# Kernel tuning notes

Hardware: AMD Instinct MI355X
Metric: run time of the kernel (lower is better)

## Reference

```python
import jax, jax.numpy as jnp
import numpy as np
from jax import lax

D_MODEL = 1024; N_HEADS = 16; D_FF = 4096
D_INNER = 2048; D_STATE = 16; D_CONV = 4; DT_RANK = 64
B = 4; T = 1024; TF = 512
HD = D_MODEL // N_HEADS


def setup_inputs() -> dict:
    key = jax.random.key(0)
    ks = jax.random.split(key, 24)
    r = lambda i, shape, s=0.02: jax.random.normal(ks[i], shape, jnp.float32) * s
    lengths = jnp.array([512, 384, 448, 320])
    styled_mask = jnp.arange(TF)[None, :] < lengths[:, None]  # True = valid
    inp = {
        'x': jax.random.normal(ks[0], (B, T, D_MODEL), jnp.float32),
        'styled_frames': jax.random.normal(ks[1], (B, TF, D_MODEL), jnp.float32),
        'styled_mask': styled_mask,
        'ln1_g': jnp.ones((D_MODEL,)), 'ln1_b': jnp.zeros((D_MODEL,)),
        'ln2_g': jnp.ones((D_MODEL,)), 'ln2_b': jnp.zeros((D_MODEL,)),
        'ln3_g': jnp.ones((D_MODEL,)), 'ln3_b': jnp.zeros((D_MODEL,)),
        'm_in_w': r(2, (D_MODEL, 2 * D_INNER)),
        'm_conv_w': r(3, (D_INNER, D_CONV), 0.1),
        'm_conv_b': jnp.zeros((D_INNER,)),
        'm_xproj_w': r(4, (D_INNER, DT_RANK + 2 * D_STATE)),
        'm_dt_w': r(5, (DT_RANK, D_INNER), 0.1),
        'm_dt_b': jnp.full((D_INNER,), -4.6),  # softplus -> dt ~ 0.01
        'm_A_log': jnp.log(jnp.broadcast_to(jnp.arange(1, D_STATE + 1, dtype=jnp.float32), (D_INNER, D_STATE))),
        'm_D': jnp.ones((D_INNER,)),
        'm_out_w': r(6, (D_INNER, D_MODEL)),
        'attn_in_w': r(7, (3 * D_MODEL, D_MODEL)),
        'attn_in_b': jnp.zeros((3 * D_MODEL,)),
        'attn_out_w': r(8, (D_MODEL, D_MODEL)),
        'attn_out_b': jnp.zeros((D_MODEL,)),
        'ff_w1': r(9, (D_MODEL, D_FF)),
        'ff_b1': jnp.zeros((D_FF,)),
        'ff_w2': r(10, (D_FF, D_MODEL)),
        'ff_b2': jnp.zeros((D_MODEL,)),
    }
    return inp


def _layer_norm(x, g, b):
    m = x.mean(-1, keepdims=True)
    v = ((x - m) ** 2).mean(-1, keepdims=True)
    return (x - m) / jnp.sqrt(v + 1e-5) * g + b


def _mamba(h, m_in_w, m_conv_w, m_conv_b, m_xproj_w, m_dt_w, m_dt_b, m_A_log, m_D, m_out_w):
    xz = h @ m_in_w                                   # (B,T,2*d_inner)
    xm, z = jnp.split(xz, 2, axis=-1)
    # causal depthwise conv1d
    xt = jnp.pad(xm.transpose(0, 2, 1), ((0, 0), (0, 0), (D_CONV - 1, 0)))  # (B,d_inner,T+pad)
    xc = lax.conv_general_dilated(xt, m_conv_w[:, None, :], (1,), 'VALID',
                                  feature_group_count=D_INNER,
                                  dimension_numbers=('NCH', 'OIH', 'NCH'))
    xc = jax.nn.silu(xc + m_conv_b[None, :, None]).transpose(0, 2, 1)       # (B,T,d_inner)
    x_dbl = xc @ m_xproj_w
    dt, Bs, Cs = jnp.split(x_dbl, [DT_RANK, DT_RANK + D_STATE], axis=-1)
    dt = jax.nn.softplus(dt @ m_dt_w + m_dt_b)        # (B,T,d_inner)
    A = -jnp.exp(m_A_log)                             # (d_inner,d_state)

    def step(hs, inp):
        dt_t, B_t, C_t, u_t = inp                     # (B,d_inner),(B,d_state),(B,d_state),(B,d_inner)
        dA = jnp.exp(dt_t[:, :, None] * A)            # (B,d_inner,d_state)
        hs = dA * hs + dt_t[:, :, None] * B_t[:, None, :] * u_t[:, :, None]
        y = jnp.einsum('bds,bs->bd', hs, C_t)
        return hs, y

    h0 = jnp.zeros((xc.shape[0], D_INNER, D_STATE), xc.dtype)
    inputs = (dt.transpose(1, 0, 2), Bs.transpose(1, 0, 2), Cs.transpose(1, 0, 2), xc.transpose(1, 0, 2))
    hT, ys = lax.scan(step, h0, inputs)
    y = ys.transpose(1, 0, 2) + xc * m_D
    y = y * jax.nn.silu(z)
    return y @ m_out_w, hT


def _cross_attn(q_in, kv_in, valid_mask, in_w, in_b, out_w, out_b):
    d = D_MODEL
    q = q_in @ in_w[:d].T + in_b[:d]
    k = kv_in @ in_w[d:2 * d].T + in_b[d:2 * d]
    v = kv_in @ in_w[2 * d:].T + in_b[2 * d:]
    q = q.reshape(q.shape[0], q.shape[1], N_HEADS, HD)
    k = k.reshape(k.shape[0], k.shape[1], N_HEADS, HD)
    v = v.reshape(v.shape[0], v.shape[1], N_HEADS, HD)
    scores = jnp.einsum('bqhd,bkhd->bhqk', q, k) / np.sqrt(HD)
    scores = jnp.where(valid_mask[:, None, None, :], scores, jnp.finfo(scores.dtype).min)
    attn = jax.nn.softmax(scores, axis=-1)
    o = jnp.einsum('bhqk,bkhd->bqhd', attn, v).reshape(q_in.shape)
    return o @ out_w.T + out_b


def reference(x, styled_frames, styled_mask,
              ln1_g, ln1_b, ln2_g, ln2_b, ln3_g, ln3_b,
              m_in_w, m_conv_w, m_conv_b, m_xproj_w, m_dt_w, m_dt_b, m_A_log, m_D, m_out_w,
              attn_in_w, attn_in_b, attn_out_w, attn_out_b,
              ff_w1, ff_b1, ff_w2, ff_b2):
    h = _layer_norm(x, ln1_g, ln1_b)
    h_mamba, new_state = _mamba(h, m_in_w, m_conv_w, m_conv_b, m_xproj_w, m_dt_w, m_dt_b, m_A_log, m_D, m_out_w)
    x = x + h_mamba
    h = _layer_norm(x, ln2_g, ln2_b)
    x = x + _cross_attn(h, styled_frames, styled_mask, attn_in_w, attn_in_b, attn_out_w, attn_out_b)
    h = _layer_norm(x, ln3_g, ln3_b)
    ff = jax.nn.gelu(h @ ff_w1 + ff_b1, approximate=False) @ ff_w2 + ff_b2
    x = x + ff
    return x, new_state
```

## Files before the change

### kernel.cpp

```cpp
#include <hip/hip_runtime.h>
#include <hip/hip_bf16.h>
#include <cstdint>

using bf16 = __hip_bfloat16;

typedef __attribute__((ext_vector_type(8))) short short8;
typedef __attribute__((ext_vector_type(4))) float floatx4;

__device__ __forceinline__ float b2f(bf16 h) { return __bfloat162float(h); }
__device__ __forceinline__ bf16 f2b(float f) { return __float2bfloat16(f); }
__device__ __forceinline__ float uitf(unsigned u) { union { unsigned u; float f; } c; c.u = u; return c.f; }

__device__ __forceinline__ void async16(const bf16* g, bf16* l) {
    __builtin_amdgcn_global_load_lds(
        (const __attribute__((address_space(1))) uint32_t*)(const void*)g,
        (__attribute__((address_space(3))) uint32_t*)(void*)l, 16, 0, 0);
}

__global__ void lens_flag_kernel(const unsigned char* __restrict__ mask,
                                 const unsigned int* __restrict__ ln1g_raw,
                                 int* __restrict__ hdr) {
    __shared__ int cnt[4];
    int tid = threadIdx.x;
    if (tid < 4) cnt[tid] = 0;
    __syncthreads();
    unsigned char b0 = mask[0], b1 = mask[1];
    int width = (b1 == 0) ? 4 : ((b0 == 1) ? 1 : 2);
    if (width == 4) {
        const unsigned int* m = (const unsigned int*)mask;
        for (int i = tid; i < 2048; i += 256) if (m[i] != 0u) atomicAdd(&cnt[i >> 9], 1);
    } else if (width == 2) {
        const unsigned short* m = (const unsigned short*)mask;
        for (int i = tid; i < 2048; i += 256) if (m[i] != 0u) atomicAdd(&cnt[i >> 9], 1);
    } else {
        for (int i = tid; i < 2048; i += 256) if (mask[i] != 0u) atomicAdd(&cnt[i >> 9], 1);
    }
    __syncthreads();
    if (tid < 4) hdr[tid] = cnt[tid];
    if (tid == 4) hdr[4] = (ln1g_raw[0] == 0x3F800000u) ? 1 : 0;
}

__global__ void convert_kernel(const void* __restrict__ src, bf16* __restrict__ dst, int n,
                               const int* __restrict__ flagp) {
    int i = blockIdx.x * 256 + threadIdx.x;
    if (i >= n) return;
    if (*flagp) dst[i] = f2b(((const float*)src)[i]);
    else        dst[i] = ((const bf16*)src)[i];
}

struct SmallSrcs { const void* p[15]; };
__global__ void convert_smalls_kernel(SmallSrcs s, bf16* __restrict__ dst,
                                      const int* __restrict__ flagp) {
    const int ends[16] = {0, 1024, 2048, 3072, 4096, 5120, 6144, 14336, 16384, 18432,
                          51200, 53248, 56320, 57344, 61440, 62464};
    int i = blockIdx.x * 256 + threadIdx.x;
    if (i >= 62464) return;
    int seg = 0;
    #pragma unroll
    for (int k = 1; k < 16; ++k) if (i >= ends[k]) seg = k;
    int local = i - ends[seg];
    const void* sp = s.p[seg];
    if (*flagp) dst[i] = f2b(((const float*)sp)[local]);
    else        dst[i] = ((const bf16*)sp)[local];
}

__global__ void transpose_any(const void* __restrict__ src, bf16* __restrict__ dst,
                              int R, int C, const int* __restrict__ flagp) {
    __shared__ bf16 tile[32][33];
    bool f32 = (*flagp != 0);
    int bx = blockIdx.x * 32, by = blockIdx.y * 32;
    int tx = threadIdx.x;
    for (int i = threadIdx.y; i < 32; i += 8) {
        int y = by + i, x = bx + tx;
        if (y < R && x < C) {
            size_t idx = (size_t)y * C + x;
            tile[i][tx] = f32 ? f2b(((const float*)src)[idx]) : ((const bf16*)src)[idx];
        }
    }
    __syncthreads();
    for (int i = threadIdx.y; i < 32; i += 8) {
        int yo = bx + i, xo = by + tx;
        if (yo < C && xo < R) dst[(size_t)yo * R + xo] = tile[tx][i];
    }
}

__global__ void vtrans_kernel(const bf16* __restrict__ kv, bf16* __restrict__ vt) {
    __shared__ bf16 t[32][33];
    int kc = blockIdx.x * 32, dc = blockIdx.y * 32;
    int bh = blockIdx.z; int b = bh >> 4, h = bh & 15;
    int tx = threadIdx.x;
    for (int i = threadIdx.y; i < 32; i += 8)
        t[i][tx] = kv[(size_t)(b * 512 + kc + i) * 2048 + 1024 + h * 64 + dc + tx];
    __syncthreads();
    for (int i = threadIdx.y; i < 32; i += 8)
        vt[(size_t)(bh * 64 + dc + i) * 512 + kc + tx] = t[tx][i];
}

__global__ __launch_bounds__(256) void ln_kernel(const bf16* __restrict__ x, const bf16* __restrict__ g,
                                                 const bf16* __restrict__ bb, bf16* __restrict__ out) {
    int row = blockIdx.x, tid = threadIdx.x;
    const bf16* xr = x + (size_t)row * 1024;
    float v[4];
    {
        uint2 raw = *(const uint2*)(xr + tid * 4);
        v[0] = uitf(raw.x << 16); v[1] = uitf(raw.x & 0xffff0000u);
        v[2] = uitf(raw.y << 16); v[3] = uitf(raw.y & 0xffff0000u);
    }
    float sum = v[0] + v[1] + v[2] + v[3];
    float sq = v[0]*v[0] + v[1]*v[1] + v[2]*v[2] + v[3]*v[3];
    for (int off = 32; off; off >>= 1) { sum += __shfl_xor(sum, off); sq += __shfl_xor(sq, off); }
    __shared__ float wsm[8];
    int wave = tid >> 6;
    if ((tid & 63) == 0) { wsm[wave * 2] = sum; wsm[wave * 2 + 1] = sq; }
    __syncthreads();
    sum = wsm[0] + wsm[2] + wsm[4] + wsm[6];
    sq  = wsm[1] + wsm[3] + wsm[5] + wsm[7];
    float mean = sum * (1.f / 1024.f);
    float var = sq * (1.f / 1024.f) - mean * mean;
    float rstd = rsqrtf(var + 1e-5f);
    bf16* orow = out + (size_t)row * 1024;
    #pragma unroll
    for (int c = 0; c < 4; ++c) {
        int col = tid * 4 + c;
        orow[col] = f2b((v[c] - mean) * rstd * b2f(g[col]) + b2f(bb[col]));
    }
}

template<int BN>
__global__ __launch_bounds__(256) void gemm_bt(
    const bf16* __restrict__ A, int lda,
    const bf16* __restrict__ Bt, int ldb,
    void* __restrict__ Cp, int ldc, int c_f32,
    int M, int N, int K,
    const bf16* __restrict__ bias,
    const bf16* __restrict__ res, int ldres,
    int act)
{
    constexpr int NJ = BN / 32;
    __shared__ __align__(16) bf16 As[3][128 * 32];
    __shared__ __align__(16) bf16 Bs[3][BN * 32];
    const int tid = threadIdx.x;
    const int lane = tid & 63;
    const int wave = tid >> 6;
    const int wr = (wave >> 1) * 64;
    const int wc = (wave & 1) * (BN / 2);
    const int lrow = lane & 15;
    const int quad = lane >> 4;

    const int gx = gridDim.x;
    const int nwg = gx * gridDim.y;
    const int orig = blockIdx.y * gx + blockIdx.x;
    int wgid = orig;
    if ((nwg & 7) == 0) wgid = (orig & 7) * (nwg >> 3) + (orig >> 3);
    const int n0 = (wgid % gx) * BN;
    const int m0 = (wgid / gx) * 128;

    const int r0 = tid >> 2;
    const int c0 = (((tid & 3) ^ ((r0 >> 1) & 3)) << 3);

    floatx4 acc[4][NJ];
    #pragma unroll
    for (int i = 0; i < 4; ++i)
        #pragma unroll
        for (int j = 0; j < NJ; ++j) acc[i][j] = (floatx4){0.f, 0.f, 0.f, 0.f};

    const int n1 = n0 + r0, n2 = n0 + r0 + 64;
    const bool fullN = (n0 + BN <= N);
    const bool bok1 = n1 < N, bok2 = n2 < N;
    const int4 z4 = {0, 0, 0, 0};

    const bf16* Ag1 = A + (size_t)(m0 + r0) * lda + c0;
    const bf16* Ag2 = A + (size_t)(m0 + r0 + 64) * lda + c0;
    const bf16* Bg1 = Bt + (size_t)n1 * ldb + c0;
    const bf16* Bg2 = Bt + (size_t)n2 * ldb + c0;

    const int chsw = ((quad ^ ((lrow >> 1) & 3)) << 3);
    const int nt = K >> 5;

    if (fullN) {
        auto stage = [&](int buf, int k0) {
            bf16* AsW = &As[buf][tid * 8];
            bf16* BsW = &Bs[buf][tid * 8];
            async16(Ag1 + k0, AsW);
            async16(Ag2 + k0, AsW + 64 * 32);
            async16(Bg1 + k0, BsW);
            if constexpr (BN == 128) async16(Bg2 + k0, BsW + 64 * 32);
        };
        const unsigned asB0 = (unsigned)(uintptr_t)(void*)&As[0][0];
        const unsigned bsB0 = (unsigned)(uintptr_t)(void*)&Bs[0][0];
        unsigned aoff[4], boff[NJ];
        #pragma unroll
        for (int i = 0; i < 4; ++i) aoff[i] = asB0 + (unsigned)(((wr + i * 16 + lrow) * 32 + chsw) * 2);
        #pragma unroll
        for (int j = 0; j < NJ; ++j) boff[j] = bsB0 + (unsigned)(((wc + j * 16 + lrow) * 32 + chsw) * 2);

        stage(0, 0);
        if (nt > 1) stage(1, 32);
        int cur = 0;
        for (int t = 0; t < nt; ++t) {
            if (t + 1 < nt) {
                if constexpr (BN == 128) asm volatile("s_waitcnt vmcnt(4)" ::: "memory");
                else                     asm volatile("s_waitcnt vmcnt(3)" ::: "memory");
            } else {
                asm volatile("s_waitcnt vmcnt(0)" ::: "memory");
            }
            __builtin_amdgcn_s_barrier();
            __builtin_amdgcn_sched_barrier(0);
            if (t + 2 < nt) {
                int nb = cur + 2; if (nb >= 3) nb -= 3;
                stage(nb, (t + 2) << 5);
            }
            const unsigned abuf = (unsigned)(cur * 128 * 32 * 2);
            const unsigned bbuf = (unsigned)(cur * BN * 32 * 2);
            short8 af[4], bfr[NJ];
            #pragma unroll
            for (int i = 0; i < 4; ++i)
                asm volatile("ds_read_b128 %0, %1" : "=v"(af[i]) : "v"(aoff[i] + abuf));
            #pragma unroll
            for (int j = 0; j < NJ; ++j)
                asm volatile("ds_read_b128 %0, %1" : "=v"(bfr[j]) : "v"(boff[j] + bbuf));
            asm volatile("s_waitcnt lgkmcnt(0)" ::: "memory");
            __builtin_amdgcn_sched_barrier(0);
            #pragma unroll
            for (int i = 0; i < 4; ++i)
                #pragma unroll
                for (int j = 0; j < NJ; ++j)
                    acc[i][j] = __builtin_amdgcn_mfma_f32_16x16x32_bf16(af[i], bfr[j], acc[i][j], 0, 0, 0);
            if (++cur == 3) cur = 0;
        }
    } else {
        bf16* AsW = &As[0][tid * 8];
        bf16* BsW = &Bs[0][tid * 8];
        for (int k0 = 0; k0 < K; k0 += 32) {
            __syncthreads();
            async16(Ag1 + k0, AsW);
            async16(Ag2 + k0, AsW + 64 * 32);
            *(int4*)BsW = bok1 ? *(const int4*)(Bg1 + k0) : z4;
            if constexpr (BN == 128)
                *(int4*)(BsW + 64 * 32) = bok2 ? *(const int4*)(Bg2 + k0) : z4;
            __syncthreads();
            short8 af[4], bfr[NJ];
            #pragma unroll
            for (int i = 0; i < 4; ++i) af[i]  = *(const short8*)&As[0][(wr + i * 16 + lrow) * 32 + chsw];
            #pragma unroll
            for (int j = 0; j < NJ; ++j) bfr[j] = *(const short8*)&Bs[0][(wc + j * 16 + lrow) * 32 + chsw];
            #pragma unroll
            for (int i = 0; i < 4; ++i)
                #pragma unroll
                for (int j = 0; j < NJ; ++j)
                    acc[i][j] = __builtin_amdgcn_mfma_f32_16x16x32_bf16(af[i], bfr[j], acc[i][j], 0, 0, 0);
        }
    }

    #pragma unroll
    for (int j = 0; j < NJ; ++j) {
        int col = n0 + wc + j * 16 + lrow;
        if (col >= N) continue;
        float bv = bias ? b2f(bias[col]) : 0.f;
        #pragma unroll
        for (int i = 0; i < 4; ++i) {
            #pragma unroll
            for (int r = 0; r < 4; ++r) {
                int row = m0 + wr + i * 16 + quad * 4 + r;
                float v = acc[i][j][r] + bv;
                if (act == 1)      v = 0.5f * v * (1.f + erff(v * 0.70710678118f));
                else if (act == 2) v = (v > 15.f) ? v : log1pf(__expf(v));
                if (res) v += b2f(res[(size_t)row * ldres + col]);
                if (c_f32) ((float*)Cp)[(size_t)row * ldc + col] = v;
                else       ((bf16*)Cp)[(size_t)row * ldc + col] = f2b(v);
            }
        }
    }
}

__global__ __launch_bounds__(256) void conv_silu_kernel(const bf16* __restrict__ xz, const bf16* __restrict__ cw,
                                                        const bf16* __restrict__ cb, bf16* __restrict__ xc) {
    int idx = blockIdx.x * 256 + threadIdx.x;
    int d = idx & 2047;
    int row = idx >> 11;
    int t = row & 1023;
    int base = row - t;
    float acc = b2f(cb[d]);
    #pragma unroll
    for (int j = 0; j < 4; ++j) {
        int tt = t - 3 + j;
        if (tt >= 0) acc += b2f(xz[(size_t)(base + tt) * 4096 + d]) * b2f(cw[d * 4 + j]);
    }
    xc[idx] = f2b(acc * (1.f / (1.f + __expf(-acc))));
}

__global__ __launch_bounds__(256) void scan_part1(
    const bf16* __restrict__ dt, const bf16* __restrict__ xc, const bf16* __restrict__ xdbl,
    const bf16* __restrict__ A_log, float* __restrict__ Pb, float* __restrict__ qb)
{
    __shared__ float smB[128][20];
    const int tid = threadIdx.x;
    const int dgrp = blockIdx.x, c = blockIdx.y, b = blockIdx.z;
    const int dl = tid >> 1, sh = tid & 1;
    const int d = (dgrp << 7) + dl;
    const size_t rowbase = (size_t)b * 1024 + (size_t)c * 128;

    {
        int r = tid >> 1, q = tid & 1;
        short8 raw = *(const short8*)(xdbl + (rowbase + r) * 96 + 64 + q * 8);
        #pragma unroll
        for (int j = 0; j < 8; ++j) smB[r][q * 8 + j] = b2f(((const bf16*)&raw)[j]);
    }
    __syncthreads();

    float A2[8], h[8];
    #pragma unroll
    for (int s = 0; s < 8; ++s) {
        A2[s] = -__expf(b2f(A_log[d * 16 + sh * 8 + s])) * 1.44269504f;
        h[s] = 0.f;
    }
    float dtsum = 0.f;
    const bf16* dtp = dt + rowbase * 2048 + d;
    const bf16* up  = xc + rowbase * 2048 + d;
    for (int tc = 0; tc < 128; tc += 8) {
        float dtv[8], uv[8];
        #pragma unroll
        for (int i = 0; i < 8; ++i) {
            dtv[i] = b2f(dtp[(size_t)(tc + i) * 2048]);
            uv[i]  = b2f(up[(size_t)(tc + i) * 2048]);
        }
        #pragma unroll
        for (int i = 0; i < 8; ++i) {
            float dtf = dtv[i];
            dtsum += dtf;
            float w = dtf * uv[i];
            float4 B0 = *(const float4*)&smB[tc + i][sh * 8];
            float4 B1 = *(const float4*)&smB[tc + i][sh * 8 + 4];
            float Bv[8] = {B0.x, B0.y, B0.z, B0.w, B1.x, B1.y, B1.z, B1.w};
            #pragma unroll
            for (int s = 0; s < 8; ++s) {
                float e = __builtin_amdgcn_exp2f(dtf * A2[s]);
                h[s] = fmaf(e, h[s], w * Bv[s]);
            }
        }
    }
    size_t gid = ((size_t)(b * 2048 + d) * 16 + sh * 8) + (size_t)c * 131072;
    float Pv[8];
    #pragma unroll
    for (int s = 0; s < 8; ++s) Pv[s] = __builtin_amdgcn_exp2f(A2[s] * dtsum);
    *(float4*)(Pb + gid)     = *(float4*)&Pv[0];
    *(float4*)(Pb + gid + 4) = *(float4*)&Pv[4];
    *(float4*)(qb + gid)     = *(float4*)&h[0];
    *(float4*)(qb + gid + 4) = *(float4*)&h[4];
}

__global__ __launch_bounds__(256) void scan_stitch(
    const float* __restrict__ Pb, const float* __restrict__ qb,
    float* __restrict__ hs, float* __restrict__ state_out)
{
    int gid = blockIdx.x * 256 + threadIdx.x;
    float h = 0.f;
    #pragma unroll
    for (int c = 0; c < 8; ++c) {
        hs[gid + c * 131072] = h;
        h = Pb[gid + c * 131072] * h + qb[gid + c * 131072];
    }
    state_out[gid] = h;
}

__global__ __launch_bounds__(256) void scan_part3(
    const bf16* __restrict__ dt, const bf16* __restrict__ xc, const bf16* __restrict__ xdbl,
    const bf16* __restrict__ xz, const bf16* __restrict__ A_log, const bf16* __restrict__ Dp,
    const float* __restrict__ hs, bf16* __restrict__ ymul)
{
    __shared__ float smBC[128][36];
    const int tid = threadIdx.x;
    const int dgrp = blockIdx.x, c = blockIdx.y, b = blockIdx.z;
    const int dl = tid >> 1, sh = tid & 1;
    const int d = (dgrp << 7) + dl;
    const size_t rowbase = (size_t)b * 1024 + (size_t)c * 128;

    {
        int r = tid >> 1, q = tid & 1;
        const bf16* src = xdbl + (rowbase + r) * 96 + 64 + q * 16;
        short8 raw0 = *(const short8*)src;
        short8 raw1 = *(const short8*)(src + 8);
        #pragma unroll
        for (int j = 0; j < 8; ++j) {
            smBC[r][q * 16 + j]     = b2f(((const bf16*)&raw0)[j]);
            smBC[r][q * 16 + 8 + j] = b2f(((const bf16*)&raw1)[j]);
        }
    }
    __syncthreads();

    float A2[8], h[8];
    size_t gid = ((size_t)(b * 2048 + d) * 16 + sh * 8) + (size_t)c * 131072;
    {
        float4 h0 = *(const float4*)(hs + gid);
        float4 h1 = *(const float4*)(hs + gid + 4);
        h[0] = h0.x; h[1] = h0.y; h[2] = h0.z; h[3] = h0.w;
        h[4] = h1.x; h[5] = h1.y; h[6] = h1.z; h[7] = h1.w;
    }
    #pragma unroll
    for (int s = 0; s < 8; ++s)
        A2[s] = -__expf(b2f(A_log[d * 16 + sh * 8 + s])) * 1.44269504f;
    const float Dv = b2f(Dp[d]);
    const bf16* dtp = dt + rowbase * 2048 + d;
    const bf16* up  = xc + rowbase * 2048 + d;
    const bf16* zp  = xz + rowbase * 4096 + 2048 + d;
    bf16* yp = ymul + rowbase * 2048 + d;
    for (int tc = 0; tc < 128; tc += 8) {
        float dtv[8], uv[8], zv[8];
        #pragma unroll
        for (int i = 0; i < 8; ++i) {
            dtv[i] = b2f(dtp[(size_t)(tc + i) * 2048]);
            uv[i]  = b2f(up[(size_t)(tc + i) * 2048]);
            zv[i]  = b2f(zp[(size_t)(tc + i) * 4096]);
        }
        #pragma unroll
        for (int i = 0; i < 8; ++i) {
            float dtf = dtv[i], uf = uv[i];
            float w = dtf * uf;
            float4 B0 = *(const float4*)&smBC[tc + i][sh * 8];
            float4 B1 = *(const float4*)&smBC[tc + i][sh * 8 + 4];
            float4 C0 = *(const float4*)&smBC[tc + i][16 + sh * 8];
            float4 C1 = *(const float4*)&smBC[tc + i][16 + sh * 8 + 4];
            float Bv[8] = {B0.x, B0.y, B0.z, B0.w, B1.x, B1.y, B1.z, B1.w};
            float Cv[8] = {C0.x, C0.y, C0.z, C0.w, C1.x, C1.y, C1.z, C1.w};
            float y = 0.f;
            #pragma unroll
            for (int s = 0; s < 8; ++s) {
                float e = __builtin_amdgcn_exp2f(dtf * A2[s]);
                h[s] = fmaf(e, h[s], w * Bv[s]);
                y = fmaf(h[s], Cv[s], y);
            }
            y += __shfl_xor(y, 1);
            float z = zv[i];
            float sig = __builtin_amdgcn_rcpf(1.f + __builtin_amdgcn_exp2f(-1.44269504f * z));
            float o = (y + uf * Dv) * (z * sig);
            if (sh == 0) yp[(size_t)(tc + i) * 2048] = f2b(o);
        }
    }
}

__global__ __launch_bounds__(256) void attn_mfma(
    const bf16* __restrict__ qb, const bf16* __restrict__ kv, const bf16* __restrict__ vt,
    const int* __restrict__ lens, bf16* __restrict__ ob)
{
    const int qt = blockIdx.x, h = blockIdx.y, b = blockIdx.z;
    const int tid = threadIdx.x;
    const int wave = tid >> 6;
    const int lane = tid & 63;
    const int l15 = lane & 15;
    const int quad = lane >> 4;
    const int len = lens[b];

    __shared__ __align__(16) bf16 Ps[32][520];
    __shared__ float red_sh[4][32];

    short8 aq[2][2];
    const bf16* qbase = qb + (size_t)(b * 1024 + qt * 32 + l15) * 1024 + h * 64 + quad * 8;
    #pragma unroll
    for (int mt = 0; mt < 2; ++mt)
        #pragma unroll
        for (int ks = 0; ks < 2; ++ks)
            aq[mt][ks] = *(const short8*)(qbase + (size_t)mt * 16 * 1024 + ks * 32);

    floatx4 accs[2][8];
    #pragma unroll
    for (int mt = 0; mt < 2; ++mt)
        #pragma unroll
        for (int nt = 0; nt < 8; ++nt) accs[mt][nt] = (floatx4){0.f, 0.f, 0.f, 0.f};

    const bf16* kbase = kv + (size_t)(b * 512 + wave * 128 + l15) * 2048 + h * 64 + quad * 8;
    #pragma unroll
    for (int nt = 0; nt < 8; ++nt) {
        short8 bk0 = *(const short8*)(kbase + (size_t)nt * 16 * 2048);
        short8 bk1 = *(const short8*)(kbase + (size_t)nt * 16 * 2048 + 32);
        #pragma unroll
        for (int mt = 0; mt < 2; ++mt) {
            accs[mt][nt] = __builtin_amdgcn_mfma_f32_16x16x32_bf16(aq[mt][0], bk0, accs[mt][nt], 0, 0, 0);
            accs[mt][nt] = __builtin_amdgcn_mfma_f32_16x16x32_bf16(aq[mt][1], bk1, accs[mt][nt], 0, 0, 0);
        }
    }

    float pm[2][4];
    #pragma unroll
    for (int mt = 0; mt < 2; ++mt)
        #pragma unroll
        for (int r = 0; r < 4; ++r) pm[mt][r] = -1e30f;
    #pragma unroll
    for (int mt = 0; mt < 2; ++mt)
        #pragma unroll
        for (int nt = 0; nt < 8; ++nt) {
            int col = wave * 128 + nt * 16 + l15;
            bool ok = col < len;
            #pragma unroll
            for (int r = 0; r < 4; ++r) {
                float s = ok ? accs[mt][nt][r] * 0.125f : -1e30f;
                accs[mt][nt][r] = s;
                pm[mt][r] = fmaxf(pm[mt][r], s);
            }
        }
    #pragma unroll
    for (int off = 1; off < 16; off <<= 1)
        #pragma unroll
        for (int mt = 0; mt < 2; ++mt)
            #pragma unroll
            for (int r = 0; r < 4; ++r) pm[mt][r] = fmaxf(pm[mt][r], __shfl_xor(pm[mt][r], off));
    if (l15 == 0)
        #pragma unroll
        for (int mt = 0; mt < 2; ++mt)
            #pragma unroll
            for (int r = 0; r < 4; ++r) red_sh[wave][mt * 16 + quad * 4 + r] = pm[mt][r];
    __syncthreads();
    float rowmax[2][4];
    #pragma unroll
    for (int mt = 0; mt < 2; ++mt)
        #pragma unroll
        for (int r = 0; r < 4; ++r) {
            int row = mt * 16 + quad * 4 + r;
            rowmax[mt][r] = fmaxf(fmaxf(red_sh[0][row], red_sh[1][row]),
                                  fmaxf(red_sh[2][row], red_sh[3][row]));
        }
    __syncthreads();

    float ps[2][4] = {{0.f, 0.f, 0.f, 0.f}, {0.f, 0.f, 0.f, 0.f}};
    #pragma unroll
    for (int mt = 0; mt < 2; ++mt)
        #pragma unroll
        for (int nt = 0; nt < 8; ++nt)
            #pragma unroll
            for (int r = 0; r < 4; ++r) {
                float p = __expf(accs[mt][nt][r] - rowmax[mt][r]);
                accs[mt][nt][r] = p;
                ps[mt][r] += p;
            }
    #pragma unroll
    for (int off = 1; off < 16; off <<= 1)
        #pragma unroll
        for (int mt = 0; mt < 2; ++mt)
            #pragma unroll
            for (int r = 0; r < 4; ++r) ps[mt][r] += __shfl_xor(ps[mt][r], off);
    if (l15 == 0)
        #pragma unroll
        for (int mt = 0; mt < 2; ++mt)
            #pragma unroll
            for (int r = 0; r < 4; ++r) red_sh[wave][mt * 16 + quad * 4 + r] = ps[mt][r];
    #pragma unroll
    for (int mt = 0; mt < 2; ++mt)
        #pragma unroll
        for (int nt = 0; nt < 8; ++nt)
            #pragma unroll
            for (int r = 0; r < 4; ++r)
                Ps[mt * 16 + quad * 4 + r][wave * 128 + nt * 16 + l15] = f2b(accs[mt][nt][r]);
    __syncthreads();
    float rowsum[2][4];
    #pragma unroll
    for (int mt = 0; mt < 2; ++mt)
        #pragma unroll
        for (int r = 0; r < 4; ++r) {
            int row = mt * 16 + quad * 4 + r;
            rowsum[mt][r] = red_sh[0][row] + red_sh[1][row] + red_sh[2][row] + red_sh[3][row];
        }

    floatx4 acco[2];
    acco[0] = (floatx4){0.f, 0.f, 0.f, 0.f};
    acco[1] = (floatx4){0.f, 0.f, 0.f, 0.f};
    const bf16* vtbase = vt + (size_t)((b * 16 + h) * 64 + wave * 16 + l15) * 512 + quad * 8;
    #pragma unroll
    for (int kc = 0; kc < 16; ++kc) {
        short8 bv = *(const short8*)(vtbase + kc * 32);
        short8 ap0 = *(const short8*)&Ps[l15][kc * 32 + quad * 8];
        short8 ap1 = *(const short8*)&Ps[16 + l15][kc * 32 + quad * 8];
        acco[0] = __builtin_amdgcn_mfma_f32_16x16x32_bf16(ap0, bv, acco[0], 0, 0, 0);
        acco[1] = __builtin_amdgcn_mfma_f32_16x16x32_bf16(ap1, bv, acco[1], 0, 0, 0);
    }

    #pragma unroll
    for (int mt = 0; mt < 2; ++mt)
        #pragma unroll
        for (int r = 0; r < 4; ++r) {
            int row = b * 1024 + qt * 32 + mt * 16 + quad * 4 + r;
            int col = h * 64 + wave * 16 + l15;
            ob[(size_t)row * 1024 + col] = f2b(acco[mt][r] / rowsum[mt][r]);
        }
}

extern "C" void kernel_launch(void* const* d_in, const int* in_sizes, int n_in,
                              void* d_out, int out_size, void* d_ws, size_t ws_size,
                              hipStream_t stream) {
    bf16* W = (bf16*)d_ws;
    int* hdr = (int*)d_ws;
    const int* flagp = hdr + 4;
    const size_t CV_X     = 32;
    const size_t CV_ST    = CV_X    + 4194304;
    const size_t CV_AIW   = CV_ST   + 2097152;
    const size_t CV_AOW   = CV_AIW  + 3145728;
    const size_t CV_SM    = CV_AOW  + 1048576;
    const size_t WT_IN    = CV_SM   + 62464;
    const size_t WT_XPROJ = WT_IN   + 4194304;
    const size_t WT_DT    = WT_XPROJ + 196608;
    const size_t WT_OUT   = WT_DT   + 131072;
    const size_t WT_FF1   = WT_OUT  + 2097152;
    const size_t WT_FF2   = WT_FF1  + 4194304;
    const size_t HB   = WT_FF2 + 4194304;
    const size_t XZ   = HB     + 4194304;
    const size_t XC   = XZ     + 16777216;
    const size_t XDBL = XC     + 8388608;
    const size_t DTB  = XDBL   + 393216;
    const size_t YM   = DTB    + 8388608;
    const size_t X2  = HB;
    const size_t HB2 = DTB;
    const size_t Qb  = XZ;
    const size_t KV  = XZ + 4194304;
    const size_t AO  = XC;
    const size_t VT  = XC + 4194304;
    const size_t X3  = YM;
    const size_t HB3 = DTB;
    const size_t FFH = XZ;
    float* Pb = (float*)(W + HB);
    float* qbuf = Pb + 1048576;
    float* hstart = (float*)(W + WT_IN);
    const size_t S_LN1G = 0, S_LN1B = 1024, S_LN2G = 2048, S_LN2B = 3072, S_LN3G = 4096, S_LN3B = 5120;
    const size_t S_CW = 6144, S_CB = 14336, S_DTB = 16384, S_AL = 18432, S_D = 51200;
    const size_t S_AIB = 53248, S_AOB = 56320, S_FB1 = 57344, S_FB2 = 61440;

    float* out = (float*)d_out;
    float* state_out = out + (size_t)4 * 1024 * 1024;

    lens_flag_kernel<<<1, 256, 0, stream>>>((const unsigned char*)d_in[2],
                                            (const unsigned int*)d_in[3], hdr);
    convert_kernel<<<16384, 256, 0, stream>>>(d_in[0],  W + CV_X,   4194304, flagp);
    convert_kernel<<<8192,  256, 0, stream>>>(d_in[1],  W + CV_ST,  2097152, flagp);
    convert_kernel<<<12288, 256, 0, stream>>>(d_in[18], W + CV_AIW, 3145728, flagp);
    convert_kernel<<<4096,  256, 0, stream>>>(d_in[20], W + CV_AOW, 1048576, flagp);
    SmallSrcs ss;
    ss.p[0] = d_in[3];  ss.p[1] = d_in[4];  ss.p[2] = d_in[5];  ss.p[3] = d_in[6];
    ss.p[4] = d_in[7];  ss.p[5] = d_in[8];  ss.p[6] = d_in[10]; ss.p[7] = d_in[11];
    ss.p[8] = d_in[14]; ss.p[9] = d_in[15]; ss.p[10] = d_in[16]; ss.p[11] = d_in[19];
    ss.p[12] = d_in[21]; ss.p[13] = d_in[23]; ss.p[14] = d_in[25];
    convert_smalls_kernel<<<245, 256, 0, stream>>>(ss, W + CV_SM, flagp);

    dim3 tb(32, 8);
    transpose_any<<<dim3(128, 32), tb, 0, stream>>>(d_in[9],  W + WT_IN,    1024, 4096, flagp);
    transpose_any<<<dim3(3, 64),   tb, 0, stream>>>(d_in[12], W + WT_XPROJ, 2048, 96,   flagp);
    transpose_any<<<dim3(64, 2),   tb, 0, stream>>>(d_in[13], W + WT_DT,    64,   2048, flagp);
    transpose_any<<<dim3(32, 64),  tb, 0, stream>>>(d_in[17], W + WT_OUT,   2048, 1024, flagp);
    transpose_any<<<dim3(128, 32), tb, 0, stream>>>(d_in[22], W + WT_FF1,   1024, 4096, flagp);
    transpose_any<<<dim3(32, 128), tb, 0, stream>>>(d_in[24], W + WT_FF2,   4096, 1024, flagp);

    auto gemm = [&](const bf16* A, int lda, const bf16* Bt, int ldb, void* C, int ldc, int c_f32,
                    int M, int N, int K, const bf16* bias, const bf16* res, int ldres, int act) {
        if ((N & 127) == 0 && N <= 2048) {
            dim3 grid(N / 64, M / 128);
            gemm_bt<64><<<grid, 256, 0, stream>>>(A, lda, Bt, ldb, C, ldc, c_f32, M, N, K, bias, res, ldres, act);
        } else {
            dim3 grid((N + 127) / 128, M / 128);
            gemm_bt<128><<<grid, 256, 0, stream>>>(A, lda, Bt, ldb, C, ldc, c_f32, M, N, K, bias, res, ldres, act);
        }
    };

    ln_kernel<<<4096, 256, 0, stream>>>(W + CV_X, W + CV_SM + S_LN1G, W + CV_SM + S_LN1B, W + HB);
    gemm(W + HB, 1024, W + WT_IN, 1024, W + XZ, 4096, 0, 4096, 4096, 1024, nullptr, nullptr, 0, 0);
    conv_silu_kernel<<<32768, 256, 0, stream>>>(W + XZ, W + CV_SM + S_CW, W + CV_SM + S_CB, W + XC);
    gemm(W + XC, 2048, W + WT_XPROJ, 2048, W + XDBL, 96, 0, 4096, 96, 2048, nullptr, nullptr, 0, 0);
    gemm(W + XDBL, 96, W + WT_DT, 64, W + DTB, 2048, 0, 4096, 2048, 64, W + CV_SM + S_DTB, nullptr, 0, 2);
    scan_part1<<<dim3(16, 8, 4), 256, 0, stream>>>(W + DTB, W + XC, W + XDBL, W + CV_SM + S_AL, Pb, qbuf);
    scan_stitch<<<512, 256, 0, stream>>>(Pb, qbuf, hstart, state_out);
    scan_part3<<<dim3(16, 8, 4), 256, 0, stream>>>(W + DTB, W + XC, W + XDBL, W + XZ,
                                                   W + CV_SM + S_AL, W + CV_SM + S_D, hstart, W + YM);
    gemm(W + YM, 2048, W + WT_OUT, 2048, W + X2, 1024, 0, 4096, 1024, 2048, nullptr, W + CV_X, 1024, 0);

    ln_kernel<<<4096, 256, 0, stream>>>(W + X2, W + CV_SM + S_LN2G, W + CV_SM + S_LN2B, W + HB2);
    gemm(W + HB2, 1024, W + CV_AIW, 1024, W + Qb, 1024, 0, 4096, 1024, 1024, W + CV_SM + S_AIB, nullptr, 0, 0);
    gemm(W + CV_ST, 1024, W + CV_AIW + 1048576, 1024, W + KV, 2048, 0, 2048, 2048, 1024, W + CV_SM + S_AIB + 1024, nullptr, 0, 0);
    vtrans_kernel<<<dim3(16, 2, 64), tb, 0, stream>>>(W + KV, W + VT);
    attn_mfma<<<dim3(32, 16, 4), 256, 0, stream>>>(W + Qb, W + KV, W + VT, hdr, W + AO);
    gemm(W + AO, 1024, W + CV_AOW, 1024, W + X3, 1024, 0, 4096, 1024, 1024, W + CV_SM + S_AOB, W + X2, 1024, 0);

    ln_kernel<<<4096, 256, 0, stream>>>(W + X3, W + CV_SM + S_LN3G, W + CV_SM + S_LN3B, W + HB3);
    gemm(W + HB3, 1024, W + WT_FF1, 1024, W + FFH, 4096, 0, 4096, 4096, 1024, W + CV_SM + S_FB1, nullptr, 0, 1);
    gemm(W + FFH, 4096, W + WT_FF2, 4096, out, 1024, 1, 4096, 1024, 4096, W + CV_SM + S_FB2, W + X3, 1024, 0);
}
```

Baseline: 924.2 us.

## Swap MFMA operands for row-contiguous vectorized epilogue stores; drop inline-asm LDS reads

The MFMA operands are swapped so each lane's accumulator holds four consecutive columns of one row instead of four rows of one column. The epilogue can then do vectorized 8-byte bf16 or 16-byte fp32 stores and residual loads, with a scalar fallback at the N boundary. The hand-written ds_read_b128 inline assembly and its explicit lgkmcnt wait are replaced with plain C++ LDS loads, leaving scheduling to the compiler. That may change how well LDS reads overlap with MFMA work.

After: 899.1 us. -2.7%, faster.

```diff
diff --git a/kernel.cpp b/kernel.cpp
--- a/kernel.cpp
+++ b/kernel.cpp
@@ -186,14 +186,6 @@
             async16(Bg1 + k0, BsW);
             if constexpr (BN == 128) async16(Bg2 + k0, BsW + 64 * 32);
         };
-        const unsigned asB0 = (unsigned)(uintptr_t)(void*)&As[0][0];
-        const unsigned bsB0 = (unsigned)(uintptr_t)(void*)&Bs[0][0];
-        unsigned aoff[4], boff[NJ];
-        #pragma unroll
-        for (int i = 0; i < 4; ++i) aoff[i] = asB0 + (unsigned)(((wr + i * 16 + lrow) * 32 + chsw) * 2);
-        #pragma unroll
-        for (int j = 0; j < NJ; ++j) boff[j] = bsB0 + (unsigned)(((wc + j * 16 + lrow) * 32 + chsw) * 2);
-
         stage(0, 0);
         if (nt > 1) stage(1, 32);
         int cur = 0;
@@ -210,22 +202,16 @@
                 int nb = cur + 2; if (nb >= 3) nb -= 3;
                 stage(nb, (t + 2) << 5);
             }
-            const unsigned abuf = (unsigned)(cur * 128 * 32 * 2);
-            const unsigned bbuf = (unsigned)(cur * BN * 32 * 2);
             short8 af[4], bfr[NJ];
             #pragma unroll
-            for (int i = 0; i < 4; ++i)
-                asm volatile("ds_read_b128 %0, %1" : "=v"(af[i]) : "v"(aoff[i] + abuf));
-            #pragma unroll
-            for (int j = 0; j < NJ; ++j)
-                asm volatile("ds_read_b128 %0, %1" : "=v"(bfr[j]) : "v"(boff[j] + bbuf));
-            asm volatile("s_waitcnt lgkmcnt(0)" ::: "memory");
-            __builtin_amdgcn_sched_barrier(0);
+            for (int i = 0; i < 4; ++i) af[i]  = *(const short8*)&As[cur][(wr + i * 16 + lrow) * 32 + chsw];
+            #pragma unroll
+            for (int j = 0; j < NJ; ++j) bfr[j] = *(const short8*)&Bs[cur][(wc + j * 16 + lrow) * 32 + chsw];
             #pragma unroll
             for (int i = 0; i < 4; ++i)
                 #pragma unroll
                 for (int j = 0; j < NJ; ++j)
-                    acc[i][j] = __builtin_amdgcn_mfma_f32_16x16x32_bf16(af[i], bfr[j], acc[i][j], 0, 0, 0);
+                    acc[i][j] = __builtin_amdgcn_mfma_f32_16x16x32_bf16(bfr[j], af[i], acc[i][j], 0, 0, 0);
             if (++cur == 3) cur = 0;
         }
     } else {
@@ -248,26 +234,47 @@
             for (int i = 0; i < 4; ++i)
                 #pragma unroll
                 for (int j = 0; j < NJ; ++j)
-                    acc[i][j] = __builtin_amdgcn_mfma_f32_16x16x32_bf16(af[i], bfr[j], acc[i][j], 0, 0, 0);
-        }
-    }
-
-    #pragma unroll
-    for (int j = 0; j < NJ; ++j) {
-        int col = n0 + wc + j * 16 + lrow;
-        if (col >= N) continue;
-        float bv = bias ? b2f(bias[col]) : 0.f;
-        #pragma unroll
-        for (int i = 0; i < 4; ++i) {
+                    acc[i][j] = __builtin_amdgcn_mfma_f32_16x16x32_bf16(bfr[j], af[i], acc[i][j], 0, 0, 0);
+        }
+    }
+
+    #pragma unroll
+    for (int i = 0; i < 4; ++i) {
+        const int row = m0 + wr + i * 16 + lrow;
+        #pragma unroll
+        for (int j = 0; j < NJ; ++j) {
+            const int col = n0 + wc + j * 16 + quad * 4;
+            float v4[4];
             #pragma unroll
             for (int r = 0; r < 4; ++r) {
-                int row = m0 + wr + i * 16 + quad * 4 + r;
-                float v = acc[i][j][r] + bv;
+                float v = acc[i][j][r];
+                if (bias) v += b2f(bias[col + r]);
                 if (act == 1)      v = 0.5f * v * (1.f + erff(v * 0.70710678118f));
                 else if (act == 2) v = (v > 15.f) ? v : log1pf(__expf(v));
-                if (res) v += b2f(res[(size_t)row * ldres + col]);
-                if (c_f32) ((float*)Cp)[(size_t)row * ldc + col] = v;
-                else       ((bf16*)Cp)[(size_t)row * ldc + col] = f2b(v);
+                v4[r] = v;
+            }
+            if (col + 4 <= N) {
+                if (res) {
+                    uint2 rr = *(const uint2*)(res + (size_t)row * ldres + col);
+                    v4[0] += uitf(rr.x << 16); v4[1] += uitf(rr.x & 0xffff0000u);
+                    v4[2] += uitf(rr.y << 16); v4[3] += uitf(rr.y & 0xffff0000u);
+                }
+                if (c_f32) {
+                    float4 o = {v4[0], v4[1], v4[2], v4[3]};
+                    *(float4*)((float*)Cp + (size_t)row * ldc + col) = o;
+                } else {
+                    bf16 o[4] = {f2b(v4[0]), f2b(v4[1]), f2b(v4[2]), f2b(v4[3])};
+                    *(uint2*)((bf16*)Cp + (size_t)row * ldc + col) = *(uint2*)o;
+                }
+            } else {
+                #pragma unroll
+                for (int r = 0; r < 4; ++r) {
+                    if (col + r >= N) continue;
+                    float v = v4[r];
+                    if (res) v += b2f(res[(size_t)row * ldres + col + r]);
+                    if (c_f32) ((float*)Cp)[(size_t)row * ldc + col + r] = v;
+                    else       ((bf16*)Cp)[(size_t)row * ldc + col + r] = f2b(v);
+                }
             }
         }
     }
```
